# Optimization experiments

Hardware: AMD Instinct MI355X
Metric: run time of the kernel (lower is better)

The kernel has to match this reference:

```python
import jax, jax.numpy as jnp
import numpy as np

DIM = 512
HEADS = 8
HD = 64
FFN = 2048
WIN = 64            # cantor_local_window; also medium-scale stride
N_LOCAL = 64        # budget 128 * 0.5
N_MED = 38          # budget 128 * 0.3
N_GLOB = 26         # remainder (ratio 0.2)
EPS = 1e-5


def _indices(S):
    # Multi-scale O(n) sampling pattern: per-query key indices [S, K].
    pos = jnp.arange(S)[:, None]
    local = jnp.clip(pos + jnp.arange(N_LOCAL) - N_LOCAL // 2, 0, S - 1)
    med_off = (jnp.arange(N_MED) - N_MED // 2) * WIN
    medium = jnp.clip(pos + med_off, 0, S - 1)
    glob = jnp.linspace(0, S - 1, N_GLOB).astype(jnp.int32)
    glob = jnp.broadcast_to(glob[None, :], (S, N_GLOB))
    return jnp.concatenate([local, medium, glob], axis=1)


def _layernorm(x, g, b):
    mu = jnp.mean(x, axis=-1, keepdims=True)
    var = jnp.mean((x - mu) ** 2, axis=-1, keepdims=True)
    return (x - mu) * jax.lax.rsqrt(var + EPS) * g + b


def _cantor_attention(x, mask, wqkv, bqkv, wo, bo):
    B, S, D = x.shape
    qkv = x @ wqkv + bqkv                      # [B,S,3D]
    q, k, v = jnp.split(qkv, 3, axis=-1)
    heads = lambda t: t.reshape(B, S, HEADS, HD).transpose(0, 2, 1, 3)
    q, k, v = heads(q), heads(k), heads(v)     # [B,H,S,hd]
    idx = _indices(S)                          # [S,K]
    k_g = k[:, :, idx, :]                      # [B,H,S,K,hd]
    v_g = v[:, :, idx, :]
    scores = jnp.einsum('bhsd,bhskd->bhsk', q, k_g) / np.sqrt(HD).astype(np.float32)
    m_g = mask[:, idx]                         # [B,S,K]
    scores = jnp.where(m_g[:, None, :, :], scores, jnp.finfo(scores.dtype).min)
    attn = jax.nn.softmax(scores, axis=-1)
    out = jnp.einsum('bhsk,bhskd->bhsd', attn, v_g)
    out = out.transpose(0, 2, 1, 3).reshape(B, S, D)
    return out @ wo + bo


def setup_inputs() -> dict:
    key = jax.random.key(0)
    ks = jax.random.split(key, 8)
    s = lambda fan: 1.0 / np.sqrt(fan)
    return {
        'x': jax.random.normal(ks[0], (1, 2048, DIM), jnp.float32),
        'attention_mask': jnp.ones((1, 2048), jnp.bool_),
        'ln1_g': jnp.ones((DIM,), jnp.float32),
        'ln1_b': jnp.zeros((DIM,), jnp.float32),
        'ln2_g': jnp.ones((DIM,), jnp.float32),
        'ln2_b': jnp.zeros((DIM,), jnp.float32),
        'wqkv': jax.random.normal(ks[1], (DIM, 3 * DIM), jnp.float32) * s(DIM),
        'bqkv': jnp.zeros((3 * DIM,), jnp.float32),
        'wo': jax.random.normal(ks[2], (DIM, DIM), jnp.float32) * s(DIM),
        'bo': jnp.zeros((DIM,), jnp.float32),
        'w1': jax.random.normal(ks[3], (DIM, FFN), jnp.float32) * s(DIM),
        'b1': jnp.zeros((FFN,), jnp.float32),
        'w2': jax.random.normal(ks[4], (FFN, DIM), jnp.float32) * s(FFN),
        'b2': jnp.zeros((DIM,), jnp.float32),
    }


def reference(x, attention_mask, ln1_g, ln1_b, ln2_g, ln2_b,
              wqkv, bqkv, wo, bo, w1, b1, w2, b2):
    # pre-norm transformer block with Cantor O(n) attention (eval mode, dropout=0)
    attn_out = _cantor_attention(_layernorm(x, ln1_g, ln1_b), attention_mask,
                                 wqkv, bqkv, wo, bo)
    x = x + attn_out
    h = _layernorm(x, ln2_g, ln2_b)
    h = jax.nn.gelu(h @ w1 + b1, approximate=False) @ w2 + b2
    return x + h
```

## Files before the change

kernel.cpp:

```cpp
#include <hip/hip_runtime.h>
#include <math.h>

typedef float f32x4 __attribute__((ext_vector_type(4)));
typedef short s16x8 __attribute__((ext_vector_type(8)));
typedef unsigned short u16x8 __attribute__((ext_vector_type(8)));
typedef unsigned short ushort_t;
typedef unsigned int uint_t;

#define D_MODEL 512
#define N_HEADS 8
#define HEAD_D  64
#define D_FFN   2048

__device__ __forceinline__ float bf2f(unsigned short u) {
  union { unsigned int i; float f; } c; c.i = ((unsigned int)u) << 16; return c.f;
}
__device__ __forceinline__ unsigned short f2bf(float f) {
  union { float f; unsigned int i; } c; c.f = f;
  unsigned int x = c.i;
  return (unsigned short)((x + 0x7FFFu + ((x >> 16) & 1u)) >> 16);
}
__device__ __forceinline__ float ldx(const void* p, size_t i, int f) {
  return f ? ((const float*)p)[i] : bf2f(((const ushort_t*)p)[i]);
}

struct DetectArgs { const void* p[14]; int n[14]; };

__global__ __launch_bounds__(256)
void detect_all(DetectArgs a, int* __restrict__ flags) {
  __shared__ int cnt[2];
  const int b = blockIdx.x;
  const int t = threadIdx.x;
  if (b == 1) { if (t == 0) flags[1] = 0; return; }
  if (t == 0) { cnt[0] = 0; cnt[1] = 0; }
  __syncthreads();
  const int n_u32 = a.n[b] >> 1;
  const int sample = n_u32 < 256 ? n_u32 : 256;
  if (t < sample) {
    uint_t u = ((const uint_t*)a.p[b])[t];
    if (u != 0u) {
      atomicAdd(&cnt[0], 1);
      int e = (u >> 7) & 0xFF;
      if (e >= 0x70 && e <= 0x83) atomicAdd(&cnt[1], 1);
    }
  }
  __syncthreads();
  if (t == 0) flags[b] = (cnt[0] >= 32 && cnt[1] * 4 <= cnt[0]) ? 1 : 0;
}

struct WDesc { const void* src; ushort_t* dst; int Kd, Nd, flag, tile0; };

__global__ __launch_bounds__(256)
void prep_kernel(WDesc w0, WDesc w1, WDesc w2, WDesc w3, int nconv,
                 const void* __restrict__ x, const void* __restrict__ g,
                 const void* __restrict__ b, ushort_t* __restrict__ h1,
                 const int* __restrict__ flags) {
  __shared__ ushort_t tile[32][33];
  const int blk = blockIdx.x;
  if (blk >= nconv) {
    const int fx = flags[0], fg = flags[2], fb = flags[3];
    const int row = (blk - nconv) * 4 + (threadIdx.x >> 6);
    const int lane = threadIdx.x & 63;
    float v[8], sum = 0.f, sq = 0.f;
#pragma unroll
    for (int i = 0; i < 8; ++i) {
      v[i] = ldx(x, (size_t)row * D_MODEL + lane * 8 + i, fx);
      sum += v[i]; sq += v[i] * v[i];
    }
#pragma unroll
    for (int o = 32; o > 0; o >>= 1) { sum += __shfl_xor(sum, o); sq += __shfl_xor(sq, o); }
    const float mu = sum * (1.0f / D_MODEL);
    const float var = sq * (1.0f / D_MODEL) - mu * mu;
    const float rstd = rsqrtf(var + 1e-5f);
#pragma unroll
    for (int i = 0; i < 8; ++i) {
      int c = lane * 8 + i;
      h1[(size_t)row * D_MODEL + c] =
          f2bf((v[i] - mu) * rstd * ldx(g, c, fg) + ldx(b, c, fb));
    }
    return;
  }
  WDesc d = (blk < w1.tile0) ? w0 : (blk < w2.tile0) ? w1 : (blk < w3.tile0) ? w2 : w3;
  const int lt = blk - d.tile0;
  const int tn = d.Nd / 32;
  const int bk = lt / tn, bn = lt % tn;
  const int f = flags[d.flag];
  const int tx = threadIdx.x & 31, ty = threadIdx.x >> 5;
#pragma unroll
  for (int r = 0; r < 4; ++r) {
    int k = bk * 32 + ty * 4 + r;
    tile[ty * 4 + r][tx] = f2bf(ldx(d.src, (size_t)k * d.Nd + bn * 32 + tx, f));
  }
  __syncthreads();
#pragma unroll
  for (int r = 0; r < 4; ++r) {
    int n = bn * 32 + ty * 4 + r;
    d.dst[(size_t)n * d.Kd + bk * 32 + tx] = tile[tx][ty * 4 + r];
  }
}

__global__ __launch_bounds__(256)
void ln1_kernel(const void* __restrict__ x, const void* __restrict__ g,
                const void* __restrict__ b, ushort_t* __restrict__ out,
                const int* __restrict__ flags) {
  const int fx = flags[0], fg = flags[2], fb = flags[3];
  const int row = blockIdx.x * 4 + (threadIdx.x >> 6);
  const int lane = threadIdx.x & 63;
  float v[8], sum = 0.f, sq = 0.f;
#pragma unroll
  for (int i = 0; i < 8; ++i) {
    v[i] = ldx(x, (size_t)row * D_MODEL + lane * 8 + i, fx);
    sum += v[i]; sq += v[i] * v[i];
  }
#pragma unroll
  for (int o = 32; o > 0; o >>= 1) { sum += __shfl_xor(sum, o); sq += __shfl_xor(sq, o); }
  const float mu = sum * (1.0f / D_MODEL);
  const float var = sq * (1.0f / D_MODEL) - mu * mu;
  const float rstd = rsqrtf(var + 1e-5f);
#pragma unroll
  for (int i = 0; i < 8; ++i) {
    int c = lane * 8 + i;
    out[(size_t)row * D_MODEL + c] =
        f2bf((v[i] - mu) * rstd * ldx(g, c, fg) + ldx(b, c, fb));
  }
}

__global__ __launch_bounds__(256)
void ln2_kernel(const float* __restrict__ y, const void* __restrict__ g,
                const void* __restrict__ b, ushort_t* __restrict__ out,
                const int* __restrict__ flags) {
  const int fg = flags[4], fb = flags[5];
  const int row = blockIdx.x * 4 + (threadIdx.x >> 6);
  const int lane = threadIdx.x & 63;
  float v[8], sum = 0.f, sq = 0.f;
#pragma unroll
  for (int i = 0; i < 8; ++i) {
    v[i] = y[(size_t)row * D_MODEL + lane * 8 + i];
    sum += v[i]; sq += v[i] * v[i];
  }
#pragma unroll
  for (int o = 32; o > 0; o >>= 1) { sum += __shfl_xor(sum, o); sq += __shfl_xor(sq, o); }
  const float mu = sum * (1.0f / D_MODEL);
  const float var = sq * (1.0f / D_MODEL) - mu * mu;
  const float rstd = rsqrtf(var + 1e-5f);
#pragma unroll
  for (int i = 0; i < 8; ++i) {
    int c = lane * 8 + i;
    out[(size_t)row * D_MODEL + c] =
        f2bf((v[i] - mu) * rstd * ldx(g, c, fg) + ldx(b, c, fb));
  }
}

template <int BM, int BN, int EPI>
__global__ __launch_bounds__(256)
void gemm_bt(const ushort_t* __restrict__ A, int lda,
             const ushort_t* __restrict__ BT, int ldb, int K,
             const void* __restrict__ bias, int bias_off,
             const void* __restrict__ res,
             float* __restrict__ yacc,
             ushort_t* __restrict__ out_bf, int ldo,
             const int* __restrict__ flags, int ibias, int ires, int addb) {
  constexpr int BK = 64;
  constexpr int FM = BM / 32, FN = BN / 32;
  constexpr int AG = BM / 32, BG = BN / 32;
  __shared__ __attribute__((aligned(16))) ushort_t As[2][BM][64];
  __shared__ __attribute__((aligned(16))) ushort_t Bs[2][BN][64];

  const int t = threadIdx.x;
  const int lane = t & 63, wave = t >> 6;
  const int wm = wave >> 1, wn = wave & 1;
  const int q = lane >> 4, lm = lane & 15;
  const int m0 = blockIdx.y * BM, n0 = blockIdx.x * BN;
  const int srow = t >> 3, sslot = t & 7;
  const int wslot = (sslot ^ (srow & 7)) * 8;
  const int xorg = lm & 7;

  f32x4 acc[FM][FN];
#pragma unroll
  for (int i = 0; i < FM; ++i)
#pragma unroll
    for (int j = 0; j < FN; ++j) acc[i][j] = (f32x4)(0.0f);

  u16x8 av[AG], bv[BG];

  auto gload = [&](int k0) {
#pragma unroll
    for (int r = 0; r < AG; ++r)
      av[r] = *(const u16x8*)(A + (size_t)(m0 + r * 32 + srow) * lda + k0 + sslot * 8);
#pragma unroll
    for (int r = 0; r < BG; ++r)
      bv[r] = *(const u16x8*)(BT + (size_t)(n0 + r * 32 + srow) * ldb + k0 + sslot * 8);
  };
  auto swrite = [&](int buf) {
#pragma unroll
    for (int r = 0; r < AG; ++r) *(u16x8*)&As[buf][r * 32 + srow][wslot] = av[r];
#pragma unroll
    for (int r = 0; r < BG; ++r) *(u16x8*)&Bs[buf][r * 32 + srow][wslot] = bv[r];
  };
  auto frag_mfma = [&](int buf, int kh) {
    s16x8 af[FM], bf[FN];
    const int rcol = ((kh * 4 + q) ^ xorg) * 8;
#pragma unroll
    for (int i = 0; i < FM; ++i)
      af[i] = *(const s16x8*)&As[buf][wm * (BM / 2) + i * 16 + lm][rcol];
#pragma unroll
    for (int j = 0; j < FN; ++j)
      bf[j] = *(const s16x8*)&Bs[buf][wn * (BN / 2) + j * 16 + lm][rcol];
#pragma unroll
    for (int i = 0; i < FM; ++i)
#pragma unroll
      for (int j = 0; j < FN; ++j)
        acc[i][j] = __builtin_amdgcn_mfma_f32_16x16x32_bf16(af[i], bf[j], acc[i][j], 0, 0, 0);
  };

  const int NT = K / BK;
  gload(0);
  swrite(0);
  __syncthreads();
  gload(BK);
  int buf = 0;
  for (int kt = 1; kt < NT; ++kt) {
    swrite(buf ^ 1);
    if (kt + 1 < NT) gload((kt + 1) * BK);
    frag_mfma(buf, 0);
    frag_mfma(buf, 1);
    __syncthreads();
    buf ^= 1;
  }
  frag_mfma(buf, 0);
  frag_mfma(buf, 1);

  const int fbias = flags[ibias];
#pragma unroll
  for (int i = 0; i < FM; ++i) {
#pragma unroll
    for (int j = 0; j < FN; ++j) {
      const int colg = n0 + wn * (BN / 2) + j * 16 + lm;
      float bb = 0.0f;
      if (EPI <= 2 || addb) bb = ldx(bias, bias_off + colg, fbias);
#pragma unroll
      for (int r = 0; r < 4; ++r) {
        const int rowg = m0 + wm * (BM / 2) + i * 16 + q * 4 + r;
        float v = acc[i][j][r] + bb;
        const size_t off = (size_t)rowg * ldo + colg;
        if constexpr (EPI == 0) {
          out_bf[off] = f2bf(v);
        } else if constexpr (EPI == 1) {
          out_bf[off] = f2bf(0.5f * v * (1.0f + erff(v * 0.70710678f)));
        } else if constexpr (EPI == 2) {
          yacc[off] = v + ldx(res, off, flags[ires]);
        } else if constexpr (EPI == 3) {
          yacc[off] += v;
        } else {
          float fin = yacc[off] + v;
          if (flags[ires]) ((float*)(void*)out_bf)[off] = fin;
          else             out_bf[off] = f2bf(fin);
        }
      }
    }
  }
}

template <int BM, int BN, int EPI>
__global__ __launch_bounds__(256)
void gemm_nn(const ushort_t* __restrict__ A, int lda, int K,
             const void* __restrict__ B, int ldb, int brow0, int bcol0,
             const void* __restrict__ bias, int bias_off,
             const void* __restrict__ res,
             float* __restrict__ yacc,
             ushort_t* __restrict__ out_bf, int ldo,
             const int* __restrict__ flags, int iB, int ibias, int ires, int addb) {
  constexpr int BK = 32;
  constexpr int FM = BM / 32, FN = BN / 32;
  __shared__ __attribute__((aligned(16))) ushort_t As[BM][40];
  __shared__ ushort_t Bs[BK][BN + 2];
  const int t = threadIdx.x;
  const int lane = t & 63, wave = t >> 6;
  const int wm = wave >> 1, wn = wave & 1;
  const int m0 = blockIdx.y * BM, n0 = blockIdx.x * BN;
  const int fB = flags[iB], fbias = flags[ibias];
  f32x4 acc[FM][FN];
#pragma unroll
  for (int i = 0; i < FM; ++i)
#pragma unroll
    for (int j = 0; j < FN; ++j) acc[i][j] = (f32x4)(0.0f);
  const int q = lane >> 4, lm = lane & 15;
  const int arow_s = t >> 2, aslot = t & 3;
  for (int k0 = 0; k0 < K; k0 += BK) {
    __syncthreads();
#pragma unroll
    for (int r = 0; r < BM / 64; ++r) {
      int row = r * 64 + arow_s;
      *(u16x8*)&As[row][aslot * 8] =
          *(const u16x8*)(A + (size_t)(m0 + row) * lda + k0 + aslot * 8);
    }
#pragma unroll
    for (int e = 0; e < (BK * BN) / 256; ++e) {
      int id = e * 256 + t;
      int k = id / BN, n = id % BN;
      Bs[k][n] = f2bf(ldx(B, (size_t)(brow0 + k0 + k) * ldb + bcol0 + n0 + n, fB));
    }
    __syncthreads();
    s16x8 af[FM], bf[FN];
#pragma unroll
    for (int i = 0; i < FM; ++i)
      af[i] = *(const s16x8*)&As[wm * (BM / 2) + i * 16 + lm][q * 8];
#pragma unroll
    for (int j = 0; j < FN; ++j) {
      int nl = wn * (BN / 2) + j * 16 + lm;
      u16x8 tmp;
#pragma unroll
      for (int f = 0; f < 8; ++f) tmp[f] = Bs[q * 8 + f][nl];
      bf[j] = __builtin_bit_cast(s16x8, tmp);
    }
#pragma unroll
    for (int i = 0; i < FM; ++i)
#pragma unroll
      for (int j = 0; j < FN; ++j)
        acc[i][j] = __builtin_amdgcn_mfma_f32_16x16x32_bf16(af[i], bf[j], acc[i][j], 0, 0, 0);
  }
#pragma unroll
  for (int i = 0; i < FM; ++i) {
#pragma unroll
    for (int j = 0; j < FN; ++j) {
      const int col = wn * (BN / 2) + j * 16 + lm;
      float bb = 0.0f;
      if (EPI != 3 || addb) bb = ldx(bias, bias_off + n0 + col, fbias);
#pragma unroll
      for (int r = 0; r < 4; ++r) {
        const int rowg = m0 + wm * (BM / 2) + i * 16 + q * 4 + r;
        float v = acc[i][j][r] + bb;
        if constexpr (EPI == 0) {
          out_bf[(size_t)rowg * ldo + n0 + col] = f2bf(v);
        } else if constexpr (EPI == 1) {
          out_bf[(size_t)rowg * ldo + n0 + col] =
              f2bf(0.5f * v * (1.0f + erff(v * 0.70710678f)));
        } else if constexpr (EPI == 2) {
          const size_t off = (size_t)rowg * D_MODEL + n0 + col;
          yacc[off] = v + ldx(res, off, flags[ires]);
        } else {
          const size_t off = (size_t)rowg * D_MODEL + n0 + col;
          yacc[off] += v;
        }
      }
    }
  }
}

__device__ __forceinline__ int key_index(int s, int j, int S) {
  int p;
  if (j < 64)       p = s + j - 32;
  else if (j < 102) p = s + (j - 83) * 64;
  else              p = ((j - 102) * (S - 1)) / 25;
  return min(max(p, 0), S - 1);
}

__global__ __launch_bounds__(256, 4)
void attn_kernel(const ushort_t* __restrict__ qkv, ushort_t* __restrict__ out, int S) {
  const int wave = threadIdx.x >> 6, lane = threadIdx.x & 63;
  const int nb = gridDim.x;
  int bid = blockIdx.x;
  if ((nb & 7) == 0) bid = (bid & 7) * (nb >> 3) + (bid >> 3);
  const int pair = bid * 4 + wave;
  const int h = pair / S;
  const int s = pair - h * S;
  const int g = lane >> 3, d8 = (lane & 7) * 8;

  int koff[16];
#pragma unroll
  for (int r = 0; r < 16; ++r)
    koff[r] = key_index(s, r * 8 + g, S) * (3 * D_MODEL);

  u16x8 qv8 = *(const u16x8*)(qkv + (size_t)s * (3 * D_MODEL) + h * HEAD_D + d8);
  float qf[8];
#pragma unroll
  for (int e = 0; e < 8; ++e) qf[e] = bf2f(qv8[e]);

  const ushort_t* kbase = qkv + D_MODEL + h * HEAD_D + d8;
  float pr[16];
  {
    u16x8 kv[8];
#pragma unroll
    for (int r = 0; r < 8; ++r) kv[r] = *(const u16x8*)(kbase + koff[r]);
#pragma unroll
    for (int r = 0; r < 16; ++r) {
      u16x8 cur = kv[r & 7];
      if (r < 8) kv[r & 7] = *(const u16x8*)(kbase + koff[r + 8]);
      float d = 0.f;
#pragma unroll
      for (int e = 0; e < 8; ++e) d += qf[e] * bf2f(cur[e]);
      d += __shfl_xor(d, 1);
      d += __shfl_xor(d, 2);
      d += __shfl_xor(d, 4);
      pr[r] = d * 0.125f;
    }
  }

  float mx = pr[0];
#pragma unroll
  for (int r = 1; r < 16; ++r) mx = fmaxf(mx, pr[r]);
#pragma unroll
  for (int m = 8; m <= 32; m <<= 1) mx = fmaxf(mx, __shfl_xor(mx, m));
  float sm = 0.f;
#pragma unroll
  for (int r = 0; r < 16; ++r) { pr[r] = __expf(pr[r] - mx); sm += pr[r]; }
#pragma unroll
  for (int m = 8; m <= 32; m <<= 1) sm += __shfl_xor(sm, m);
  const float inv = 1.0f / sm;

  const ushort_t* vbase = qkv + 2 * D_MODEL + h * HEAD_D + d8;
  float oacc[8];
#pragma unroll
  for (int e = 0; e < 8; ++e) oacc[e] = 0.f;
  {
    u16x8 vv[8];
#pragma unroll
    for (int r = 0; r < 8; ++r) vv[r] = *(const u16x8*)(vbase + koff[r]);
#pragma unroll
    for (int r = 0; r < 16; ++r) {
      u16x8 cv = vv[r & 7];
      float cp = pr[r] * inv;
      if (r < 8) vv[r & 7] = *(const u16x8*)(vbase + koff[r + 8]);
#pragma unroll
      for (int e = 0; e < 8; ++e) oacc[e] += cp * bf2f(cv[e]);
    }
  }
#pragma unroll
  for (int m = 8; m <= 32; m <<= 1)
#pragma unroll
    for (int e = 0; e < 8; ++e) oacc[e] += __shfl_xor(oacc[e], m);

  if (lane < 8) {
    u16x8 ov;
#pragma unroll
    for (int e = 0; e < 8; ++e) ov[e] = f2bf(oacc[e]);
    *(u16x8*)(out + (size_t)s * D_MODEL + h * HEAD_D + d8) = ov;
  }
}

__global__ __launch_bounds__(256)
void convert_kernel(const float* __restrict__ y, void* __restrict__ out,
                    const int* __restrict__ flags, int n) {
  const int fout = flags[0];
  int i = blockIdx.x * 256 + threadIdx.x;
  if (i < n) {
    float v = y[i];
    if (fout) ((float*)out)[i] = v;
    else      ((ushort_t*)out)[i] = f2bf(v);
  }
}

extern "C" void kernel_launch(void* const* d_in, const int* in_sizes, int n_in,
                              void* d_out, int out_size, void* d_ws, size_t ws_size,
                              hipStream_t stream) {
  const int S = in_sizes[0] / D_MODEL;
  const size_t sD = (size_t)S * D_MODEL;
  char* ws = (char*)d_ws;

  DetectArgs da;
  for (int i = 0; i < 14; ++i) { da.p[i] = d_in[i]; da.n[i] = in_sizes[i]; }

  ushort_t* h1    = (ushort_t*)d_out;
  ushort_t* attnb = (ushort_t*)d_out;
  ushort_t* h2    = (ushort_t*)d_out;

  const size_t MB = 1024 * 1024;
  if (ws_size >= 12 * MB + 64) {
    const int P  = (ws_size >= 20 * MB) ? 1 : 2;
    const int Nc = D_FFN / P;
    char* wbase = ws + (P == 1 ? 12 : 6) * MB;

    ushort_t* qkv   = (ushort_t*)ws;
    float*    y     = (float*)ws;
    ushort_t* gbuf  = (ushort_t*)(ws + 4 * MB);
    ushort_t* wqkvT = (ushort_t*)wbase;
    ushort_t* woT   = (ushort_t*)(wbase + 1 * MB + 512 * 1024);
    ushort_t* w1T   = (ushort_t*)(wbase + 2 * MB);
    ushort_t* w2T   = (ushort_t*)(wbase + 4 * MB);
    int*      flags = (int*)(wbase + 6 * MB);

    detect_all<<<14, 256, 0, stream>>>(da, flags);

    WDesc dq  = { d_in[6],  wqkvT, D_MODEL, 3 * D_MODEL, 6,  0 };
    WDesc dwo = { d_in[8],  woT,   D_MODEL, D_MODEL,     8,  768 };
    WDesc dw1 = { d_in[10], w1T,   D_MODEL, D_FFN,       10, 1024 };
    WDesc dw2 = { d_in[12], w2T,   D_FFN,   D_MODEL,     12, 2048 };

    prep_kernel<<<3072 + S / 4, 256, 0, stream>>>(
        dq, dwo, dw1, dw2, 3072, d_in[0], d_in[2], d_in[3], h1, flags);

    gemm_bt<32, 64, 0><<<dim3(24, S / 32), 256, 0, stream>>>(
        h1, D_MODEL, wqkvT, D_MODEL, D_MODEL, d_in[7], 0,
        nullptr, nullptr, qkv, 3 * D_MODEL, flags, 7, 0, 1);

    attn_kernel<<<(S * N_HEADS) / 4, 256, 0, stream>>>(qkv, attnb, S);

    gemm_bt<32, 32, 2><<<dim3(16, S / 32), 256, 0, stream>>>(
        attnb, D_MODEL, woT, D_MODEL, D_MODEL, d_in[9], 0,
        d_in[0], y, nullptr, D_MODEL, flags, 9, 0, 1);

    ln2_kernel<<<S / 4, 256, 0, stream>>>(y, d_in[4], d_in[5], h2, flags);

    if (P == 1) {
      gemm_bt<32, 64, 1><<<dim3(D_FFN / 64, S / 32), 256, 0, stream>>>(
          h2, D_MODEL, w1T, D_MODEL, D_MODEL,
          d_in[11], 0, nullptr, nullptr, gbuf, D_FFN, flags, 11, 0, 1);
      gemm_bt<32, 32, 4><<<dim3(16, S / 32), 256, 0, stream>>>(
          gbuf, D_FFN, w2T, D_FFN, D_FFN, d_in[13], 0,
          nullptr, y, (ushort_t*)d_out, D_MODEL, flags, 13, 0, 1);
    } else {
      gemm_bt<32, 64, 1><<<dim3(Nc / 64, S / 32), 256, 0, stream>>>(
          h2, D_MODEL, w1T, D_MODEL, D_MODEL,
          d_in[11], 0, nullptr, nullptr, gbuf, Nc, flags, 11, 0, 1);
      gemm_bt<32, 32, 3><<<dim3(16, S / 32), 256, 0, stream>>>(
          gbuf, Nc, w2T, D_FFN, Nc, d_in[13], 0,
          nullptr, y, nullptr, D_MODEL, flags, 13, 0, 1);
      gemm_bt<32, 64, 1><<<dim3(Nc / 64, S / 32), 256, 0, stream>>>(
          h2, D_MODEL, w1T + (size_t)Nc * D_MODEL, D_MODEL, D_MODEL,
          d_in[11], Nc, nullptr, nullptr, gbuf, Nc, flags, 11, 0, 1);
      gemm_bt<32, 32, 4><<<dim3(16, S / 32), 256, 0, stream>>>(
          gbuf, Nc, w2T + (size_t)Nc, D_FFN, Nc, d_in[13], 0,
          nullptr, y, (ushort_t*)d_out, D_MODEL, flags, 13, 0, 0);
    }
  } else {
    int P;
    if      (ws_size >= 12ull * MB + 4096) P = 1;
    else if (ws_size >=  8ull * MB + 4096) P = 2;
    else                                   P = 4;
    const int Nc = D_FFN / P;
    const size_t gbuf_bytes = (size_t)S * Nc * 2;
    const size_t qkv_bytes  = 3 * sD * 2;
    const size_t fo = 4ull * sD + gbuf_bytes;
    const size_t flags_pos = (qkv_bytes > fo ? qkv_bytes : fo);

    ushort_t* qkv  = (ushort_t*)ws;
    float*    y    = (float*)ws;
    ushort_t* gbuf = (ushort_t*)(ws + 4 * sD);
    int*      flags = (int*)(ws + flags_pos);

    detect_all<<<14, 256, 0, stream>>>(da, flags);
    ln1_kernel<<<S / 4, 256, 0, stream>>>(d_in[0], d_in[2], d_in[3], h1, flags);
    gemm_nn<128, 128, 0><<<dim3((3 * D_MODEL) / 128, S / 128), 256, 0, stream>>>(
        h1, D_MODEL, D_MODEL, d_in[6], 3 * D_MODEL, 0, 0, d_in[7], 0,
        nullptr, nullptr, qkv, 3 * D_MODEL, flags, 6, 7, 0, 1);
    attn_kernel<<<(S * N_HEADS) / 4, 256, 0, stream>>>(qkv, attnb, S);
    gemm_nn<64, 64, 2><<<dim3(D_MODEL / 64, S / 64), 256, 0, stream>>>(
        attnb, D_MODEL, D_MODEL, d_in[8], D_MODEL, 0, 0, d_in[9], 0,
        d_in[0], y, nullptr, D_MODEL, flags, 8, 9, 0, 1);
    ln2_kernel<<<S / 4, 256, 0, stream>>>(y, d_in[4], d_in[5], h2, flags);
    for (int p = 0; p < P; ++p) {
      if (Nc >= 1024) {
        gemm_nn<128, 128, 1><<<dim3(Nc / 128, S / 128), 256, 0, stream>>>(
            h2, D_MODEL, D_MODEL, d_in[10], D_FFN, 0, p * Nc, d_in[11], p * Nc,
            nullptr, nullptr, gbuf, Nc, flags, 10, 11, 0, 1);
      } else {
        gemm_nn<64, 64, 1><<<dim3(Nc / 64, S / 64), 256, 0, stream>>>(
            h2, D_MODEL, D_MODEL, d_in[10], D_FFN, 0, p * Nc, d_in[11], p * Nc,
            nullptr, nullptr, gbuf, Nc, flags, 10, 11, 0, 1);
      }
      gemm_nn<64, 64, 3><<<dim3(D_MODEL / 64, S / 64), 256, 0, stream>>>(
          gbuf, Nc, Nc, d_in[12], D_MODEL, p * Nc, 0, d_in[13], 0,
          nullptr, y, nullptr, D_MODEL, flags, 12, 13, 0, p == 0 ? 1 : 0);
    }
    convert_kernel<<<(int)((sD + 255) / 256), 256, 0, stream>>>(y, d_out, flags, (int)sD);
  }
}
```

Baseline: 180.8 us.

## Fuse LayerNorm2 into Wo-GEMM stats and FFN1 A-operand staging

Removes the separate ln2 kernel. The Wo projection epilogue accumulates per-row sum and sum-of-squares via atomics. The FFN1 GEMM then normalizes the fp32 residual on the fly while staging A into shared memory. The LN gain is folded into W1 during weight conversion, and the LN bias is folded into a precomputed FFN1 bias (b1 + b2·W1) computed in prep_kernel. This saves one launch and the bf16 h2 round trip, at the cost of reading fp32 A in FFN1, a sequential 512-step bias dot product in prep, atomics, and a one-pass variance formula.

```diff
diff --git a/kernel.cpp b/kernel.cpp
--- a/kernel.cpp
+++ b/kernel.cpp
@@ -31,6 +31,7 @@
   __shared__ int cnt[2];
   const int b = blockIdx.x;
   const int t = threadIdx.x;
+  if (b == 0 && t == 64) flags[14] = 1;
   if (b == 1) { if (t == 0) flags[1] = 0; return; }
   if (t == 0) { cnt[0] = 0; cnt[1] = 0; }
   __syncthreads();
@@ -51,16 +52,32 @@
 struct WDesc { const void* src; ushort_t* dst; int Kd, Nd, flag, tile0; };
 
 __global__ __launch_bounds__(256)
-void prep_kernel(WDesc w0, WDesc w1, WDesc w2, WDesc w3, int nconv,
+void prep_kernel(WDesc w0, WDesc w1, WDesc w2, WDesc w3, int nconv, int nln,
                  const void* __restrict__ x, const void* __restrict__ g,
                  const void* __restrict__ b, ushort_t* __restrict__ h1,
+                 const void* __restrict__ g2, const void* __restrict__ b2,
+                 const void* __restrict__ w1src, const void* __restrict__ b1src,
+                 float* __restrict__ b1p, float* __restrict__ stats,
                  const int* __restrict__ flags) {
   __shared__ ushort_t tile[32][33];
   const int blk = blockIdx.x;
+  const int t = threadIdx.x;
+  if (blk >= nconv + nln) {
+    const int mb = blk - nconv - nln;
+    const int n = mb * 256 + t;
+    stats[n * 2] = 0.f; stats[n * 2 + 1] = 0.f;
+    const int fw1 = flags[10], fb2 = flags[5], fb1 = flags[11];
+    float acc = ldx(b1src, n, fb1);
+#pragma unroll 8
+    for (int k = 0; k < D_MODEL; ++k)
+      acc += ldx(b2, k, fb2) * ldx(w1src, (size_t)k * D_FFN + n, fw1);
+    b1p[n] = acc;
+    return;
+  }
   if (blk >= nconv) {
     const int fx = flags[0], fg = flags[2], fb = flags[3];
-    const int row = (blk - nconv) * 4 + (threadIdx.x >> 6);
-    const int lane = threadIdx.x & 63;
+    const int row = (blk - nconv) * 4 + (t >> 6);
+    const int lane = t & 63;
     float v[8], sum = 0.f, sq = 0.f;
 #pragma unroll
     for (int i = 0; i < 8; ++i) {
@@ -85,11 +102,15 @@
   const int tn = d.Nd / 32;
   const int bk = lt / tn, bn = lt % tn;
   const int f = flags[d.flag];
-  const int tx = threadIdx.x & 31, ty = threadIdx.x >> 5;
+  const int scale_w1 = (d.flag == 10 && b1p != nullptr);
+  const int fg2 = flags[4];
+  const int tx = t & 31, ty = t >> 5;
 #pragma unroll
   for (int r = 0; r < 4; ++r) {
     int k = bk * 32 + ty * 4 + r;
-    tile[ty * 4 + r][tx] = f2bf(ldx(d.src, (size_t)k * d.Nd + bn * 32 + tx, f));
+    float val = ldx(d.src, (size_t)k * d.Nd + bn * 32 + tx, f);
+    if (scale_w1) val *= ldx(g2, k, fg2);
+    tile[ty * 4 + r][tx] = f2bf(val);
   }
   __syncthreads();
 #pragma unroll
@@ -151,7 +172,7 @@
   }
 }
 
-template <int BM, int BN, int EPI>
+template <int BM, int BN, int EPI, int LNA>
 __global__ __launch_bounds__(256)
 void gemm_bt(const ushort_t* __restrict__ A, int lda,
              const ushort_t* __restrict__ BT, int ldb, int K,
@@ -159,10 +180,13 @@
              const void* __restrict__ res,
              float* __restrict__ yacc,
              ushort_t* __restrict__ out_bf, int ldo,
-             const int* __restrict__ flags, int ibias, int ires, int addb) {
+             const int* __restrict__ flags, int ibias, int ires, int addb,
+             const float* __restrict__ af32, const float* __restrict__ stats,
+             float* __restrict__ stats_out) {
   constexpr int BK = 64;
   constexpr int FM = BM / 32, FN = BN / 32;
   constexpr int AG = BM / 32, BG = BN / 32;
+  static_assert(!LNA || BM == 32, "LNA staging assumes AG==1");
   __shared__ __attribute__((aligned(16))) ushort_t As[2][BM][64];
   __shared__ __attribute__((aligned(16))) ushort_t Bs[2][BN][64];
 
@@ -182,18 +206,38 @@
     for (int j = 0; j < FN; ++j) acc[i][j] = (f32x4)(0.0f);
 
   u16x8 av[AG], bv[BG];
+  f32x4 avf0, avf1; float2 sst;
 
   auto gload = [&](int k0) {
-#pragma unroll
-    for (int r = 0; r < AG; ++r)
-      av[r] = *(const u16x8*)(A + (size_t)(m0 + r * 32 + srow) * lda + k0 + sslot * 8);
+    if constexpr (LNA) {
+      const float* yr = af32 + (size_t)(m0 + srow) * lda + k0 + sslot * 8;
+      avf0 = *(const f32x4*)yr;
+      avf1 = *(const f32x4*)(yr + 4);
+      sst = *(const float2*)&stats[(m0 + srow) * 2];
+    } else {
+#pragma unroll
+      for (int r = 0; r < AG; ++r)
+        av[r] = *(const u16x8*)(A + (size_t)(m0 + r * 32 + srow) * lda + k0 + sslot * 8);
+    }
 #pragma unroll
     for (int r = 0; r < BG; ++r)
       bv[r] = *(const u16x8*)(BT + (size_t)(n0 + r * 32 + srow) * ldb + k0 + sslot * 8);
   };
   auto swrite = [&](int buf) {
-#pragma unroll
-    for (int r = 0; r < AG; ++r) *(u16x8*)&As[buf][r * 32 + srow][wslot] = av[r];
+    if constexpr (LNA) {
+      const float mu = sst.x * (1.0f / D_MODEL);
+      const float rstd = rsqrtf(sst.y * (1.0f / D_MODEL) - mu * mu + 1e-5f);
+      u16x8 w;
+#pragma unroll
+      for (int e = 0; e < 4; ++e) {
+        w[e]     = f2bf((avf0[e] - mu) * rstd);
+        w[e + 4] = f2bf((avf1[e] - mu) * rstd);
+      }
+      *(u16x8*)&As[buf][srow][wslot] = w;
+    } else {
+#pragma unroll
+      for (int r = 0; r < AG; ++r) *(u16x8*)&As[buf][r * 32 + srow][wslot] = av[r];
+    }
 #pragma unroll
     for (int r = 0; r < BG; ++r) *(u16x8*)&Bs[buf][r * 32 + srow][wslot] = bv[r];
   };
@@ -231,6 +275,7 @@
   frag_mfma(buf, 1);
 
   const int fbias = flags[ibias];
+  float yv[4] = {0.f, 0.f, 0.f, 0.f};
 #pragma unroll
   for (int i = 0; i < FM; ++i) {
 #pragma unroll
@@ -248,13 +293,31 @@
         } else if constexpr (EPI == 1) {
           out_bf[off] = f2bf(0.5f * v * (1.0f + erff(v * 0.70710678f)));
         } else if constexpr (EPI == 2) {
-          yacc[off] = v + ldx(res, off, flags[ires]);
+          float fin = v + ldx(res, off, flags[ires]);
+          yacc[off] = fin;
+          yv[r] = fin;
         } else if constexpr (EPI == 3) {
           yacc[off] += v;
         } else {
           float fin = yacc[off] + v;
           if (flags[ires]) ((float*)(void*)out_bf)[off] = fin;
           else             out_bf[off] = f2bf(fin);
+        }
+      }
+    }
+  }
+  if constexpr (EPI == 2) {
+    static_assert(EPI != 2 || (FM == 1 && FN == 1), "stats path assumes 32x32");
+    if (stats_out) {
+#pragma unroll
+      for (int r = 0; r < 4; ++r) {
+        float s1 = yv[r], s2 = yv[r] * yv[r];
+#pragma unroll
+        for (int m = 1; m <= 8; m <<= 1) { s1 += __shfl_xor(s1, m); s2 += __shfl_xor(s2, m); }
+        if (lm == 0) {
+          const int row = m0 + wm * 16 + q * 4 + r;
+          atomicAdd(&stats_out[row * 2], s1);
+          atomicAdd(&stats_out[row * 2 + 1], s2);
         }
       }
     }
@@ -478,6 +541,8 @@
     ushort_t* w1T   = (ushort_t*)(wbase + 2 * MB);
     ushort_t* w2T   = (ushort_t*)(wbase + 4 * MB);
     int*      flags = (int*)(wbase + 6 * MB);
+    float*    stats = (float*)(wbase + 6 * MB + 1024);
+    float*    b1p   = (float*)(wbase + 6 * MB + 1024 + 16384);
 
     detect_all<<<14, 256, 0, stream>>>(da, flags);
 
@@ -486,41 +551,51 @@
     WDesc dw1 = { d_in[10], w1T,   D_MODEL, D_FFN,       10, 1024 };
     WDesc dw2 = { d_in[12], w2T,   D_FFN,   D_MODEL,     12, 2048 };
 
-    prep_kernel<<<3072 + S / 4, 256, 0, stream>>>(
-        dq, dwo, dw1, dw2, 3072, d_in[0], d_in[2], d_in[3], h1, flags);
-
-    gemm_bt<32, 64, 0><<<dim3(24, S / 32), 256, 0, stream>>>(
+    const int fuse = (P == 1);
+    prep_kernel<<<3072 + S / 4 + (fuse ? 8 : 0), 256, 0, stream>>>(
+        dq, dwo, dw1, dw2, 3072, S / 4, d_in[0], d_in[2], d_in[3], h1,
+        d_in[4], d_in[5], d_in[10], d_in[11],
+        fuse ? b1p : nullptr, stats, flags);
+
+    gemm_bt<32, 64, 0, 0><<<dim3(24, S / 32), 256, 0, stream>>>(
         h1, D_MODEL, wqkvT, D_MODEL, D_MODEL, d_in[7], 0,
-        nullptr, nullptr, qkv, 3 * D_MODEL, flags, 7, 0, 1);
+        nullptr, nullptr, qkv, 3 * D_MODEL, flags, 7, 0, 1,
+        nullptr, nullptr, nullptr);
 
     attn_kernel<<<(S * N_HEADS) / 4, 256, 0, stream>>>(qkv, attnb, S);
 
-    gemm_bt<32, 32, 2><<<dim3(16, S / 32), 256, 0, stream>>>(
+    gemm_bt<32, 32, 2, 0><<<dim3(16, S / 32), 256, 0, stream>>>(
         attnb, D_MODEL, woT, D_MODEL, D_MODEL, d_in[9], 0,
-        d_in[0], y, nullptr, D_MODEL, flags, 9, 0, 1);
-
-    ln2_kernel<<<S / 4, 256, 0, stream>>>(y, d_in[4], d_in[5], h2, flags);
+        d_in[0], y, nullptr, D_MODEL, flags, 9, 0, 1,
+        nullptr, nullptr, fuse ? stats : nullptr);
 
     if (P == 1) {
-      gemm_bt<32, 64, 1><<<dim3(D_FFN / 64, S / 32), 256, 0, stream>>>(
+      gemm_bt<32, 64, 1, 1><<<dim3(D_FFN / 64, S / 32), 256, 0, stream>>>(
+          nullptr, D_MODEL, w1T, D_MODEL, D_MODEL,
+          b1p, 0, nullptr, nullptr, gbuf, D_FFN, flags, 14, 0, 1,
+          y, stats, nullptr);
+      gemm_bt<32, 32, 4, 0><<<dim3(16, S / 32), 256, 0, stream>>>(
+          gbuf, D_FFN, w2T, D_FFN, D_FFN, d_in[13], 0,
+          nullptr, y, (ushort_t*)d_out, D_MODEL, flags, 13, 0, 1,
+          nullptr, nullptr, nullptr);
+    } else {
+      ln2_kernel<<<S / 4, 256, 0, stream>>>(y, d_in[4], d_in[5], h2, flags);
+      gemm_bt<32, 64, 1, 0><<<dim3(Nc / 64, S / 32), 256, 0, stream>>>(
           h2, D_MODEL, w1T, D_MODEL, D_MODEL,
-          d_in[11], 0, nullptr, nullptr, gbuf, D_FFN, flags, 11, 0, 1);
-      gemm_bt<32, 32, 4><<<dim3(16, S / 32), 256, 0, stream>>>(
-          gbuf, D_FFN, w2T, D_FFN, D_FFN, d_in[13], 0,
-          nullptr, y, (ushort_t*)d_out, D_MODEL, flags, 13, 0, 1);
-    } else {
-      gemm_bt<32, 64, 1><<<dim3(Nc / 64, S / 32), 256, 0, stream>>>(
-          h2, D_MODEL, w1T, D_MODEL, D_MODEL,
-          d_in[11], 0, nullptr, nullptr, gbuf, Nc, flags, 11, 0, 1);
-      gemm_bt<32, 32, 3><<<dim3(16, S / 32), 256, 0, stream>>>(
+          d_in[11], 0, nullptr, nullptr, gbuf, Nc, flags, 11, 0, 1,
+          nullptr, nullptr, nullptr);
+      gemm_bt<32, 32, 3, 0><<<dim3(16, S / 32), 256, 0, stream>>>(
           gbuf, Nc, w2T, D_FFN, Nc, d_in[13], 0,
-          nullptr, y, nullptr, D_MODEL, flags, 13, 0, 1);
-      gemm_bt<32, 64, 1><<<dim3(Nc / 64, S / 32), 256, 0, stream>>>(
+          nullptr, y, nullptr, D_MODEL, flags, 13, 0, 1,
+          nullptr, nullptr, nullptr);
+      gemm_bt<32, 64, 1, 0><<<dim3(Nc / 64, S / 32), 256, 0, stream>>>(
           h2, D_MODEL, w1T + (size_t)Nc * D_MODEL, D_MODEL, D_MODEL,
-          d_in[11], Nc, nullptr, nullptr, gbuf, Nc, flags, 11, 0, 1);
-      gemm_bt<32, 32, 4><<<dim3(16, S / 32), 256, 0, stream>>>(
+          d_in[11], Nc, nullptr, nullptr, gbuf, Nc, flags, 11, 0, 1,
+          nullptr, nullptr, nullptr);
+      gemm_bt<32, 32, 4, 0><<<dim3(16, S / 32), 256, 0, stream>>>(
           gbuf, Nc, w2T + (size_t)Nc, D_FFN, Nc, d_in[13], 0,
-          nullptr, y, (ushort_t*)d_out, D_MODEL, flags, 13, 0, 0);
+          nullptr, y, (ushort_t*)d_out, D_MODEL, flags, 13, 0, 0,
+          nullptr, nullptr, nullptr);
     }
   } else {
     int P;
```

After: 348.6 us. 1.93x slower.
